# Kernel optimization log

Measured on AMD Instinct MI355X. Metric: run time of the kernel, lower is better.

## Reference

```python
import jax, jax.numpy as jnp
import numpy as np

EPS = 1e-5          # InstanceNorm eps (torch default)
KERNEL = 25         # moving_avg_kernel_size
TAU = 1.0           # gumbel softmax temperature
REGIME_NUM = 8


def _inorm(x):
    # InstanceNorm1d without affine on (N, C, L): normalize over last dim (biased var)
    m = x.mean(-1, keepdims=True)
    v = ((x - m) ** 2).mean(-1, keepdims=True)
    return (x - m) * jax.lax.rsqrt(v + EPS)


def _lbr(x, W, b):
    # Linear -> InstanceNorm (over last dim) -> exact GELU
    return jax.nn.gelu(_inorm(x @ W + b), approximate=False)


def _moving_avg(x, k):
    # x: (B, L, C); edge-replicate pad (k-1)//2 on both sides, sliding mean via cumsum
    p = (k - 1) // 2
    xp = jnp.concatenate([jnp.repeat(x[:, :1], p, axis=1), x,
                          jnp.repeat(x[:, -1:], p, axis=1)], axis=1)
    cs = jnp.concatenate([jnp.zeros_like(xp[:, :1]), jnp.cumsum(xp, axis=1)], axis=1)
    return (cs[:, k:] - cs[:, :-k]) / k  # (B, L, C)


def _encode(x, Ws, bs, Wt, bt):
    # inputs - inputs[:, 0:1]; series decomposition; seasonal+trend branches
    x = x - x[:, :1]
    mm = _moving_avg(x, KERNEL)
    return _lbr(x - mm, Ws, bs) + _lbr(mm, Wt, bt)  # (B, L, H)


def reference(inputs_longterm, inputs_shortterm,
              Ws, bs, Wt, bt,
              Wh1, bh1, Wl1, bl1, Wh2, bh2, Wl2, bl2, Wh3, bh3, Wl3, bl3,
              Wr, br, proto):
    e_lt = _encode(inputs_longterm, Ws, bs, Wt, bt)   # (B, L_lt, H)
    e_st = _encode(inputs_shortterm, Ws, bs, Wt, bt)  # (B, L_st, H)

    # RegimeEncoder: alternate hidden-dim and lookback-dim LinearBatchRelu layers
    o = _lbr(e_lt, Wh1, bh1)
    o = jnp.swapaxes(_lbr(jnp.swapaxes(o, 1, 2), Wl1, bl1), 1, 2)
    o = _lbr(o, Wh2, bh2)
    o = jnp.swapaxes(_lbr(jnp.swapaxes(o, 1, 2), Wl2, bl2), 1, 2)
    o = _lbr(o, Wh3, bh3)
    o = jnp.swapaxes(_lbr(jnp.swapaxes(o, 1, 2), Wl3, bl3), 1, 2)  # (B, L_lt//8, H)
    logits = o.reshape(o.shape[0], -1) @ Wr + br  # (B, R)

    # gumbel_softmax(hard=True) with straight-through estimator
    g = jax.random.gumbel(jax.random.key(42), logits.shape, logits.dtype)
    y_soft = jax.nn.softmax((logits + g) / TAU, axis=-1)
    y_hard = jax.nn.one_hot(jnp.argmax(y_soft, axis=-1), REGIME_NUM, dtype=logits.dtype)
    w = y_hard - jax.lax.stop_gradient(y_soft) + y_soft  # (B, R)

    # weighted sum over regime prototypes, then combine with encoded shortterm
    sel = jnp.einsum('br,rnhmo->bnhmo', w, proto)          # (B, L_st, H, M, 3)
    out = jnp.einsum('bnh,bnhmo->bmo', e_st, sel)          # (B, M, 3)
    B = out.shape[0]
    return jax.nn.softmax(out.reshape(B, -1), axis=-1).reshape(out.shape)


def setup_inputs() -> dict:
    key = jax.random.key(0)
    ks = jax.random.split(key, 24)
    B, L_lt, L_st, C, H, R, M = 32, 512, 128, 9, 128, 8, 64
    s = 0.02
    d = {
        'inputs_longterm':  jax.random.normal(ks[0], (B, L_lt, C), jnp.float32),
        'inputs_shortterm': jax.random.normal(ks[1], (B, L_st, C), jnp.float32),
        'Ws': jax.random.normal(ks[2], (C, H), jnp.float32) * s,
        'bs': jnp.zeros((H,), jnp.float32),
        'Wt': jax.random.normal(ks[3], (C, H), jnp.float32) * s,
        'bt': jnp.zeros((H,), jnp.float32),
        'Wh1': jax.random.normal(ks[4], (H, H), jnp.float32) * s,
        'bh1': jnp.zeros((H,), jnp.float32),
        'Wl1': jax.random.normal(ks[5], (L_lt, L_lt // 2), jnp.float32) * s,
        'bl1': jnp.zeros((L_lt // 2,), jnp.float32),
        'Wh2': jax.random.normal(ks[6], (H, H), jnp.float32) * s,
        'bh2': jnp.zeros((H,), jnp.float32),
        'Wl2': jax.random.normal(ks[7], (L_lt // 2, L_lt // 4), jnp.float32) * s,
        'bl2': jnp.zeros((L_lt // 4,), jnp.float32),
        'Wh3': jax.random.normal(ks[8], (H, H), jnp.float32) * s,
        'bh3': jnp.zeros((H,), jnp.float32),
        'Wl3': jax.random.normal(ks[9], (L_lt // 4, L_lt // 8), jnp.float32) * s,
        'bl3': jnp.zeros((L_lt // 8,), jnp.float32),
        'Wr': jax.random.normal(ks[10], (H * L_lt // 8, R), jnp.float32) * s,
        'br': jnp.zeros((R,), jnp.float32),
        'proto': jax.random.normal(ks[11], (R, L_st, H, M, 3), jnp.float32),
    }
    return d
```

## Files before the change

### kernel.cpp

```cpp
#include <hip/hip_runtime.h>
#include <math.h>

#define EPS 1e-5f

__device__ __forceinline__ float gelu_exact(float x) {
    return 0.5f * x * (1.0f + erff(x * 0.7071067811865476f));
}

__device__ float block_sum(float v, float* red) {
    int lane = threadIdx.x & 63, wid = threadIdx.x >> 6;
#pragma unroll
    for (int off = 32; off > 0; off >>= 1) v += __shfl_down(v, off, 64);
    if (lane == 0) red[wid] = v;
    __syncthreads();
    int nw = ((int)blockDim.x + 63) >> 6;
    float s = red[0];
    for (int w = 1; w < nw; w++) s += red[w];
    __syncthreads();
    return s;
}

__device__ float block_max(float v, float* red) {
    int lane = threadIdx.x & 63, wid = threadIdx.x >> 6;
#pragma unroll
    for (int off = 32; off > 0; off >>= 1) v = fmaxf(v, __shfl_down(v, off, 64));
    if (lane == 0) red[wid] = v;
    __syncthreads();
    int nw = ((int)blockDim.x + 63) >> 6;
    float s = red[0];
    for (int w = 1; w < nw; w++) s = fmaxf(s, red[w]);
    __syncthreads();
    return s;
}

__device__ void threefry2x32(unsigned k0, unsigned k1, unsigned x0, unsigned x1,
                             unsigned& o0, unsigned& o1) {
    unsigned ks[3] = {k0, k1, k0 ^ k1 ^ 0x1BD11BDAu};
    const unsigned rot[2][4] = {{13u, 15u, 26u, 6u}, {17u, 29u, 16u, 24u}};
    x0 += ks[0]; x1 += ks[1];
#pragma unroll
    for (int i = 0; i < 5; i++) {
#pragma unroll
        for (int j = 0; j < 4; j++) {
            unsigned r = rot[i & 1][j];
            x0 += x1;
            x1 = (x1 << r) | (x1 >> (32 - r));
            x1 ^= x0;
        }
        x0 += ks[(i + 1) % 3];
        x1 += ks[(i + 2) % 3] + (unsigned)(i + 1);
    }
    o0 = x0; o1 = x1;
}

__device__ float gumbel_at(int j) {
    unsigned o0, o1;
    threefry2x32(0u, 42u, 0u, (unsigned)j, o0, o1);
    unsigned bits = o0 ^ o1;
    float f = __uint_as_float((bits >> 9) | 0x3F800000u) - 1.0f;
    float u = fmaxf(f + 1.17549435e-38f, 1.17549435e-38f);
    return -logf(-logf(u));
}

__device__ void bsum2_128(float& a, float& b, float (*red)[2]) {
    int lane = threadIdx.x & 63, wid = threadIdx.x >> 6;
#pragma unroll
    for (int off = 32; off > 0; off >>= 1) {
        a += __shfl_xor(a, off, 64);
        b += __shfl_xor(b, off, 64);
    }
    if (lane == 0) { red[wid][0] = a; red[wid][1] = b; }
    __syncthreads();
    a = red[0][0] + red[1][0];
    b = red[0][1] + red[1][1];
}

__global__ void encode_kernel(const float* __restrict__ x_lt, const float* __restrict__ x_st,
                              const float* __restrict__ Ws, const float* __restrict__ bs,
                              const float* __restrict__ Wt, const float* __restrict__ bt,
                              float* __restrict__ e_lt, float* __restrict__ e_st) {
    const int H = 128;
    int b = blockIdx.y, t = threadIdx.x;
    const float* x;
    float* e;
    int L, l;
    if (blockIdx.x < 512) { x = x_lt; e = e_lt; L = 512; l = blockIdx.x; }
    else { x = x_st; e = e_st; L = 128; l = blockIdx.x - 512; }
    __shared__ float part[117];
    __shared__ float seas[9], mmv[9];
    __shared__ float redA[2][2], redB[2][2];
    const float* xb = x + (size_t)b * L * 9;
    if (t < 117) {
        int c = t / 13, g = t % 13;
        int lj0 = l + 2 * g - 12;
        lj0 = lj0 < 0 ? 0 : (lj0 >= L ? L - 1 : lj0);
        float s = xb[(size_t)lj0 * 9 + c];
        if (g < 12) {
            int lj1 = l + 2 * g - 11;
            lj1 = lj1 < 0 ? 0 : (lj1 >= L ? L - 1 : lj1);
            s += xb[(size_t)lj1 * 9 + c];
        }
        part[t] = s;
    }
    __syncthreads();
    if (t < 9) {
        float s = 0.f;
        for (int g = 0; g < 13; g++) s += part[t * 13 + g];
        float x0 = xb[t];
        float mm = (s - 25.f * x0) * (1.0f / 25.0f);
        float xd = xb[(size_t)l * 9 + t] - x0;
        mmv[t] = mm;
        seas[t] = xd - mm;
    }
    __syncthreads();
    float ys = bs[t], yt = bt[t];
#pragma unroll
    for (int c = 0; c < 9; c++) {
        ys += seas[c] * Ws[c * H + t];
        yt += mmv[c] * Wt[c * H + t];
    }
    float sa = ys, sb = yt;
    bsum2_128(sa, sb, redA);
    float ms = sa * (1.0f / 128.0f), mt = sb * (1.0f / 128.0f);
    float ds = ys - ms, dt = yt - mt;
    float qa = ds * ds, qb = dt * dt;
    bsum2_128(qa, qb, redB);
    float gy = gelu_exact(ds * rsqrtf(qa * (1.0f / 128.0f) + EPS));
    float gt = gelu_exact(dt * rsqrtf(qb * (1.0f / 128.0f) + EPS));
    e[((size_t)b * L + l) * H + t] = gy + gt;
}

template <int K, int N, int WR, bool TRANS>
__global__ __launch_bounds__(256) void lbr_wave(
    const float* __restrict__ A, int S, int ABOFF,
    const float* __restrict__ W, const float* __restrict__ bias,
    float* __restrict__ out, int OROWS, int OBOFF) {
    constexpr int CG = N / 4;
    constexpr int SG = 64 / CG;
    constexpr int RW = SG * WR;
    constexpr int MT = 4 * RW;
    constexpr int LOG2MT = (MT == 8) ? 3 : ((MT == 16) ? 4 : 5);
    constexpr int STAGE = 4 * RW * K;
    constexpr int TILE = TRANS ? MT * (N + 4) : 0;
    constexpr int LSZ = STAGE > TILE ? STAGE : TILE;
    __shared__ float lds[LSZ];
    const int t = threadIdx.x;
    const int w = t >> 6, ln = t & 63;
    const int sg = ln / CG;
    const int n0 = (ln % CG) * 4;
    const int b = blockIdx.y;
    const int r0b = blockIdx.x * MT;
    const int r0w = r0b + w * RW;
    float* As = lds + w * RW * K;
    const float* Ab = A + (size_t)b * ABOFF;
    for (int idx = ln; idx < RW * (K / 4); idx += 64) {
        int rr = idx / (K / 4), kk = idx % (K / 4);
        float4 v = *(const float4*)(Ab + (size_t)(r0w + rr) * S + kk * 4);
        *(float4*)(As + rr * K + kk * 4) = v;
    }
    float4 acc[WR];
    {
        float4 bv = *(const float4*)(bias + n0);
#pragma unroll
        for (int j = 0; j < WR; j++) acc[j] = bv;
    }
    const float* ap = As + (sg * WR) * K;
    const float* wp = W + n0;
#pragma unroll 8
    for (int k = 0; k < K; k++) {
        float4 wv = *(const float4*)wp;
        wp += N;
#pragma unroll
        for (int j = 0; j < WR; j++) {
            float a = ap[j * K + k];
            acc[j].x += a * wv.x;
            acc[j].y += a * wv.y;
            acc[j].z += a * wv.z;
            acc[j].w += a * wv.w;
        }
    }
    float4 res[WR];
#pragma unroll
    for (int j = 0; j < WR; j++) {
        float s = acc[j].x + acc[j].y + acc[j].z + acc[j].w;
#pragma unroll
        for (int off = CG / 2; off > 0; off >>= 1) s += __shfl_xor(s, off, 64);
        float m = s * (1.0f / (float)N);
        float dx = acc[j].x - m, dy = acc[j].y - m, dz = acc[j].z - m, dw = acc[j].w - m;
        float q = dx * dx + dy * dy + dz * dz + dw * dw;
#pragma unroll
        for (int off = CG / 2; off > 0; off >>= 1) q += __shfl_xor(q, off, 64);
        float inv = rsqrtf(q * (1.0f / (float)N) + EPS);
        res[j].x = gelu_exact(dx * inv);
        res[j].y = gelu_exact(dy * inv);
        res[j].z = gelu_exact(dz * inv);
        res[j].w = gelu_exact(dw * inv);
    }
    if constexpr (TRANS) {
        __syncthreads();
#pragma unroll
        for (int j = 0; j < WR; j++) {
            int rl = w * RW + sg * WR + j;
            *(float4*)(lds + rl * (N + 4) + n0) = res[j];
        }
        __syncthreads();
        float* ob = out + (size_t)b * OBOFF + r0b;
        for (int e = t; e < MT * N; e += 256) {
            int r = e & (MT - 1), n = e >> LOG2MT;
            ob[(size_t)n * OROWS + r] = lds[r * (N + 4) + n];
        }
    } else {
        float* ob = out + (size_t)b * OBOFF;
#pragma unroll
        for (int j = 0; j < WR; j++) {
            int row = r0w + sg * WR + j;
            *(float4*)(ob + (size_t)row * N + n0) = res[j];
        }
    }
}

__global__ void logits_select(const float* __restrict__ O6, const float* __restrict__ Wr,
                              const float* __restrict__ br,
                              float* __restrict__ sel_w, int* __restrict__ sel_r) {
    int b = blockIdx.x, t = threadIdx.x;
    const float* ob = O6 + (size_t)b * 8192;
    float acc[8] = {0, 0, 0, 0, 0, 0, 0, 0};
#pragma unroll 4
    for (int q = 0; q < 32; q++) {
        int i = q * 256 + t;
        int l4 = i >> 7, h = i & 127;
        float v = ob[h * 64 + l4];
        const float* wr = Wr + (size_t)i * 8;
#pragma unroll
        for (int j = 0; j < 8; j++) acc[j] += v * wr[j];
    }
#pragma unroll
    for (int j = 0; j < 8; j++)
#pragma unroll
        for (int off = 32; off > 0; off >>= 1) acc[j] += __shfl_xor(acc[j], off, 64);
    __shared__ float red[4][8];
    int lane = t & 63, wid = t >> 6;
    if (lane == 0)
        for (int j = 0; j < 8; j++) red[wid][j] = acc[j];
    __syncthreads();
    if (t == 0) {
        float z[8];
        for (int j = 0; j < 8; j++) {
            float lg = br[j] + red[0][j] + red[1][j] + red[2][j] + red[3][j];
            z[j] = lg + gumbel_at(b * 8 + j);
        }
        int am = 0;
        float zm = z[0];
        for (int j = 1; j < 8; j++)
            if (z[j] > zm) { zm = z[j]; am = j; }
        float ssum = 0.f;
        for (int j = 0; j < 8; j++) ssum += expf(z[j] - zm);
        float s = 1.0f / ssum;
        sel_w[b] = (1.0f - s) + s;
        sel_r[b] = am;
    }
}

__global__ void einsum_nsplit(const float* __restrict__ e_st, const float* __restrict__ proto,
                              const int* __restrict__ sel_r, float* __restrict__ part) {
    int n = blockIdx.x, r = blockIdx.y, t = threadIdx.x;
    __shared__ int loc[32];
    __shared__ int s_gs;
    if (t == 0) {
        int g = 0;
        for (int bb = 0; bb < 32; bb++)
            if (sel_r[bb] == r) loc[g++] = bb;
        s_gs = g;
    }
    __syncthreads();
    int gs = s_gs;
    if (gs == 0) return;
    __shared__ float es[8][128];
    const float* pb = proto + ((size_t)r * 128 + n) * 128 * 192;
    for (int s0 = 0; s0 < gs; s0 += 8) {
        int np = gs - s0 < 8 ? gs - s0 : 8;
        __syncthreads();
        for (int i = t; i < 1024; i += 192) {
            int sb = i >> 7, h = i & 127;
            if (sb < np) {
                int b = loc[s0 + sb];
                es[sb][h] = e_st[((size_t)b * 128 + n) * 128 + h];
            } else {
                es[sb][h] = 0.f;
            }
        }
        __syncthreads();
        float a0 = 0.f, a1 = 0.f, a2 = 0.f, a3 = 0.f;
        float a4 = 0.f, a5 = 0.f, a6 = 0.f, a7 = 0.f;
#pragma unroll 8
        for (int h = 0; h < 128; h++) {
            float p = pb[h * 192 + t];
            a0 += es[0][h] * p; a1 += es[1][h] * p;
            a2 += es[2][h] * p; a3 += es[3][h] * p;
            a4 += es[4][h] * p; a5 += es[5][h] * p;
            a6 += es[6][h] * p; a7 += es[7][h] * p;
        }
        float av[8] = {a0, a1, a2, a3, a4, a5, a6, a7};
#pragma unroll
        for (int sb = 0; sb < 8; sb++) {
            if (sb < np) {
                int b = loc[s0 + sb];
                part[((size_t)b * 128 + n) * 192 + t] = av[sb];
            }
        }
    }
}

__global__ void finalize_kernel(const float* __restrict__ part, const float* __restrict__ sel_w,
                                float* __restrict__ out) {
    int b = blockIdx.x, t = threadIdx.x;
    __shared__ float red[4];
    float v = 0.f;
#pragma unroll 8
    for (int c = 0; c < 128; c++) v += part[((size_t)b * 128 + c) * 192 + t];
    v *= sel_w[b];
    float mx = block_max(v, red);
    float e = expf(v - mx);
    float s = block_sum(e, red);
    out[(size_t)b * 192 + t] = e / s;
}

extern "C" void kernel_launch(void* const* d_in, const int* in_sizes, int n_in,
                              void* d_out, int out_size, void* d_ws, size_t ws_size,
                              hipStream_t stream) {
    const float* in_lt = (const float*)d_in[0];
    const float* in_st = (const float*)d_in[1];
    const float* Ws  = (const float*)d_in[2];  const float* bs  = (const float*)d_in[3];
    const float* Wt  = (const float*)d_in[4];  const float* bt  = (const float*)d_in[5];
    const float* Wh1 = (const float*)d_in[6];  const float* bh1 = (const float*)d_in[7];
    const float* Wl1 = (const float*)d_in[8];  const float* bl1 = (const float*)d_in[9];
    const float* Wh2 = (const float*)d_in[10]; const float* bh2 = (const float*)d_in[11];
    const float* Wl2 = (const float*)d_in[12]; const float* bl2 = (const float*)d_in[13];
    const float* Wh3 = (const float*)d_in[14]; const float* bh3 = (const float*)d_in[15];
    const float* Wl3 = (const float*)d_in[16]; const float* bl3 = (const float*)d_in[17];
    const float* Wr  = (const float*)d_in[18]; const float* br  = (const float*)d_in[19];
    const float* proto = (const float*)d_in[20];
    float* out = (float*)d_out;

    float* ws = (float*)d_ws;
    size_t off = 0;
    float* e_lt = ws + off; off += (size_t)32 * 512 * 128;
    float* e_st = ws + off; off += (size_t)32 * 128 * 128;
    float* O1T = ws + off; off += (size_t)128 * 16384;
    float* O2T = ws + off; off += (size_t)256 * 4096;
    float* O3T = ws + off; off += (size_t)128 * 8192;
    float* O4T = ws + off; off += (size_t)128 * 4096;
    float* O5T = ws + off; off += (size_t)128 * 4096;
    float* O6 = ws + off; off += (size_t)32 * 128 * 64;
    float* part = ws + off; off += (size_t)32 * 128 * 192;
    float* sel_w = ws + off; off += 32;
    int* sel_r = (int*)(ws + off); off += 32;

    encode_kernel<<<dim3(640, 32), 128, 0, stream>>>(in_lt, in_st, Ws, bs, Wt, bt, e_lt, e_st);
    lbr_wave<128, 128, 2, true><<<dim3(1024, 1), 256, 0, stream>>>(
        e_lt, 128, 0, Wh1, bh1, O1T, 16384, 0);
    lbr_wave<512, 256, 4, true><<<dim3(8, 32), 256, 0, stream>>>(
        O1T, 16384, 512, Wl1, bl1, O2T, 4096, 128);
    lbr_wave<128, 128, 4, true><<<dim3(8, 32), 256, 0, stream>>>(
        O2T, 4096, 128, Wh2, bh2, O3T, 8192, 256);
    lbr_wave<256, 128, 2, true><<<dim3(8, 32), 256, 0, stream>>>(
        O3T, 8192, 256, Wl2, bl2, O4T, 4096, 128);
    lbr_wave<128, 128, 2, true><<<dim3(8, 32), 256, 0, stream>>>(
        O4T, 4096, 128, Wh3, bh3, O5T, 4096, 128);
    lbr_wave<128, 64, 1, false><<<dim3(8, 32), 256, 0, stream>>>(
        O5T, 4096, 128, Wl3, bl3, O6, 0, 8192);
    logits_select<<<32, 256, 0, stream>>>(O6, Wr, br, sel_w, sel_r);
    einsum_nsplit<<<dim3(128, 8), 192, 0, stream>>>(e_st, proto, sel_r, part);
    finalize_kernel<<<32, 192, 0, stream>>>(part, sel_w, out);
}
```

Measured before the change: 378.7 us.

## Vectorize LBR inner loop, stage logits in LDS, widen grids for middle layers

```diff
diff --git a/kernel.cpp b/kernel.cpp
--- a/kernel.cpp
+++ b/kernel.cpp
@@ -166,17 +166,24 @@
     }
     const float* ap = As + (sg * WR) * K;
     const float* wp = W + n0;
-#pragma unroll 8
-    for (int k = 0; k < K; k++) {
-        float4 wv = *(const float4*)wp;
-        wp += N;
+#pragma unroll 2
+    for (int k = 0; k < K; k += 4) {
+        float4 w0 = *(const float4*)(wp);
+        float4 w1 = *(const float4*)(wp + N);
+        float4 w2 = *(const float4*)(wp + 2 * N);
+        float4 w3 = *(const float4*)(wp + 3 * N);
+        wp += 4 * N;
 #pragma unroll
         for (int j = 0; j < WR; j++) {
-            float a = ap[j * K + k];
-            acc[j].x += a * wv.x;
-            acc[j].y += a * wv.y;
-            acc[j].z += a * wv.z;
-            acc[j].w += a * wv.w;
+            float4 a4 = *(const float4*)(ap + j * K + k);
+            acc[j].x += a4.x * w0.x; acc[j].y += a4.x * w0.y;
+            acc[j].z += a4.x * w0.z; acc[j].w += a4.x * w0.w;
+            acc[j].x += a4.y * w1.x; acc[j].y += a4.y * w1.y;
+            acc[j].z += a4.y * w1.z; acc[j].w += a4.y * w1.w;
+            acc[j].x += a4.z * w2.x; acc[j].y += a4.z * w2.y;
+            acc[j].z += a4.z * w2.z; acc[j].w += a4.z * w2.w;
+            acc[j].x += a4.w * w3.x; acc[j].y += a4.w * w3.y;
+            acc[j].z += a4.w * w3.z; acc[j].w += a4.w * w3.w;
         }
     }
     float4 res[WR];
@@ -219,26 +226,35 @@
     }
 }
 
-__global__ void logits_select(const float* __restrict__ O6, const float* __restrict__ Wr,
-                              const float* __restrict__ br,
-                              float* __restrict__ sel_w, int* __restrict__ sel_r) {
+__global__ __launch_bounds__(256) void logits_select(
+    const float* __restrict__ O6, const float* __restrict__ Wr,
+    const float* __restrict__ br, float* __restrict__ sel_w, int* __restrict__ sel_r) {
     int b = blockIdx.x, t = threadIdx.x;
-    const float* ob = O6 + (size_t)b * 8192;
+    __shared__ float sO6[128 * 68];
+    __shared__ float red[4][8];
+    const float4* ob4 = (const float4*)(O6 + (size_t)b * 8192);
+    for (int i4 = t; i4 < 2048; i4 += 256) {
+        float4 v = ob4[i4];
+        int p = i4 * 4;
+        int h = p >> 6, l4 = p & 63;
+        *(float4*)(&sO6[h * 68 + l4]) = v;
+    }
+    __syncthreads();
     float acc[8] = {0, 0, 0, 0, 0, 0, 0, 0};
 #pragma unroll 4
     for (int q = 0; q < 32; q++) {
         int i = q * 256 + t;
         int l4 = i >> 7, h = i & 127;
-        float v = ob[h * 64 + l4];
-        const float* wr = Wr + (size_t)i * 8;
-#pragma unroll
-        for (int j = 0; j < 8; j++) acc[j] += v * wr[j];
+        float v = sO6[h * 68 + l4];
+        const float4* wr = (const float4*)(Wr + (size_t)i * 8);
+        float4 w0 = wr[0], w1 = wr[1];
+        acc[0] += v * w0.x; acc[1] += v * w0.y; acc[2] += v * w0.z; acc[3] += v * w0.w;
+        acc[4] += v * w1.x; acc[5] += v * w1.y; acc[6] += v * w1.z; acc[7] += v * w1.w;
     }
 #pragma unroll
     for (int j = 0; j < 8; j++)
 #pragma unroll
         for (int off = 32; off > 0; off >>= 1) acc[j] += __shfl_xor(acc[j], off, 64);
-    __shared__ float red[4][8];
     int lane = t & 63, wid = t >> 6;
     if (lane == 0)
         for (int j = 0; j < 8; j++) red[wid][j] = acc[j];
@@ -280,14 +296,14 @@
     for (int s0 = 0; s0 < gs; s0 += 8) {
         int np = gs - s0 < 8 ? gs - s0 : 8;
         __syncthreads();
-        for (int i = t; i < 1024; i += 192) {
-            int sb = i >> 7, h = i & 127;
+        for (int i4 = t; i4 < 256; i4 += 192) {
+            int sb = i4 >> 5, h4 = i4 & 31;
+            float4 v = make_float4(0.f, 0.f, 0.f, 0.f);
             if (sb < np) {
                 int b = loc[s0 + sb];
-                es[sb][h] = e_st[((size_t)b * 128 + n) * 128 + h];
-            } else {
-                es[sb][h] = 0.f;
+                v = ((const float4*)(e_st + ((size_t)b * 128 + n) * 128))[h4];
             }
+            *(float4*)(&es[sb][h4 * 4]) = v;
         }
         __syncthreads();
         float a0 = 0.f, a1 = 0.f, a2 = 0.f, a3 = 0.f;
@@ -359,13 +375,13 @@
     encode_kernel<<<dim3(640, 32), 128, 0, stream>>>(in_lt, in_st, Ws, bs, Wt, bt, e_lt, e_st);
     lbr_wave<128, 128, 2, true><<<dim3(1024, 1), 256, 0, stream>>>(
         e_lt, 128, 0, Wh1, bh1, O1T, 16384, 0);
-    lbr_wave<512, 256, 4, true><<<dim3(8, 32), 256, 0, stream>>>(
+    lbr_wave<512, 256, 2, true><<<dim3(16, 32), 256, 0, stream>>>(
         O1T, 16384, 512, Wl1, bl1, O2T, 4096, 128);
-    lbr_wave<128, 128, 4, true><<<dim3(8, 32), 256, 0, stream>>>(
+    lbr_wave<128, 128, 2, true><<<dim3(16, 32), 256, 0, stream>>>(
         O2T, 4096, 128, Wh2, bh2, O3T, 8192, 256);
-    lbr_wave<256, 128, 2, true><<<dim3(8, 32), 256, 0, stream>>>(
+    lbr_wave<256, 128, 1, true><<<dim3(16, 32), 256, 0, stream>>>(
         O3T, 8192, 256, Wl2, bl2, O4T, 4096, 128);
-    lbr_wave<128, 128, 2, true><<<dim3(8, 32), 256, 0, stream>>>(
+    lbr_wave<128, 128, 1, true><<<dim3(16, 32), 256, 0, stream>>>(
         O4T, 4096, 128, Wh3, bh3, O5T, 4096, 128);
     lbr_wave<128, 64, 1, false><<<dim3(8, 32), 256, 0, stream>>>(
         O5T, 4096, 128, Wl3, bl3, O6, 0, 8192);
```

Result: faster. 362.2 us (-4.4%).
